# Kernel tuning notes

Hardware: AMD Instinct MI355X
Metric: run time of the kernel (lower is better)

The kernel has to match this reference:

```python
import jax, jax.numpy as jnp
import numpy as np

N_NODES = 50000
N_EDGES = 800000
F_IN = 128      # n_alleles
HID = 64        # ge_hidden_dim
HEADS = 2       # gat_heads
LAT = 128       # latent_dim
N_PHEN = 50


def setup_inputs() -> dict:
    key = jax.random.key(0)
    ks = jax.random.split(key, 16)
    s = 0.05
    return {
        'x': jax.random.normal(ks[0], (N_NODES, F_IN), jnp.float32),
        'edge_index': jax.random.randint(ks[1], (2, N_EDGES), 0, N_NODES, jnp.int64),
        'pheno_idx': jnp.arange(N_PHEN, dtype=jnp.int64),
        'pheno_embedding': jax.random.normal(ks[2], (N_PHEN, F_IN), jnp.float32) * 0.1,
        'Wl1': jax.random.normal(ks[3], (F_IN, HEADS * HID), jnp.float32) * s,
        'Wr1': jax.random.normal(ks[4], (F_IN, HEADS * HID), jnp.float32) * s,
        'att1': jax.random.normal(ks[5], (HEADS, HID), jnp.float32) * s,
        'b1': jax.random.normal(ks[6], (HEADS * HID,), jnp.float32) * s,
        'Wl2': jax.random.normal(ks[7], (HEADS * HID, LAT), jnp.float32) * s,
        'Wr2': jax.random.normal(ks[8], (HEADS * HID, LAT), jnp.float32) * s,
        'att2': jax.random.normal(ks[9], (1, LAT), jnp.float32) * s,
        'b2': jax.random.normal(ks[10], (LAT,), jnp.float32) * s,
        'Wp': jax.random.normal(ks[11], (LAT, LAT), jnp.float32) * s,
        'bp': jax.random.normal(ks[12], (LAT,), jnp.float32) * s,
    }


def gatv2_conv(x, src, dst, Wl, Wr, att, bias, concat):
    # PyG GATv2Conv: e = att . leaky_relu(Wl x_src + Wr x_dst, 0.2), softmax over dst
    N = x.shape[0]
    H, C = att.shape
    xl = (x @ Wl).reshape(N, H, C)
    xr = (x @ Wr).reshape(N, H, C)
    feat = jax.nn.leaky_relu(xl[src] + xr[dst], 0.2)         # [E,H,C]
    logits = jnp.einsum('ehc,hc->eh', feat, att)             # [E,H]
    m = jax.ops.segment_max(logits, dst, num_segments=N)     # [N,H]
    ex = jnp.exp(logits - m[dst])
    denom = jax.ops.segment_sum(ex, dst, num_segments=N)
    alpha = ex / denom[dst]                                  # [E,H]
    out = jax.ops.segment_sum(alpha[:, :, None] * xl[src], dst, num_segments=N)
    out = out.reshape(N, H * C) if concat else out.mean(axis=1)
    return out + bias


def reference(x, edge_index, pheno_idx, pheno_embedding,
              Wl1, Wr1, att1, b1, Wl2, Wr2, att2, b2, Wp, bp):
    N = x.shape[0]
    # learnable phenotype node embeddings replace their input features
    x = x.at[pheno_idx].set(pheno_embedding)
    # PyG default: add self loops
    loops = jnp.arange(N, dtype=edge_index.dtype)
    src = jnp.concatenate([edge_index[0], loops])
    dst = jnp.concatenate([edge_index[1], loops])
    h = jax.nn.leaky_relu(gatv2_conv(x, src, dst, Wl1, Wr1, att1, b1, True), 0.01)
    h = gatv2_conv(h, src, dst, Wl2, Wr2, att2, b2, False)
    graph_embedding = h[pheno_idx].mean(axis=0, keepdims=True)  # [1, LAT]
    return graph_embedding @ Wp + bp
```

## Files before the change

kernel.cpp:

```cpp
#include <hip/hip_runtime.h>
#include <hip/hip_fp16.h>
#include <cstdint>

#define F_DIM 128

__device__ __forceinline__ float lrelu(float x, float s) { return x > 0.f ? x : s * x; }

template<int W>
__device__ __forceinline__ float redg(float p) {
  #pragma unroll
  for (int d = 1; d < W; d <<= 1) p += __shfl_xor(p, d);
  return p;
}

__device__ __forceinline__ int cidx(const int* __restrict__ csr, int k, int last) {
  return csr[k <= last ? k : last];
}

__device__ __forceinline__ __half2 shfl_xor_h2(__half2 v, int m) {
  union { __half2 h; int i; } u; u.h = v;
  u.i = __shfl_xor(u.i, m);
  return u.h;
}

typedef _Float16 h2v __attribute__((ext_vector_type(2)));
__device__ __forceinline__ __half2 h2max(__half2 a, __half2 b) {
  union { __half2 h; h2v v; } ua, ub, ur;
  ua.h = a; ub.h = b;
  ur.v = __builtin_elementwise_max(ua.v, ub.v);
  return ur.h;
}

union H2U { __half2 h[2]; uint2 u; };

__global__ void k_init(int* __restrict__ deg, int* __restrict__ rowmap, int N) {
  int i = blockIdx.x * blockDim.x + threadIdx.x;
  if (i < N) { deg[i] = 0; rowmap[i] = -1; }
}

__global__ void k_hist_rowmap(const int* __restrict__ dst, int* __restrict__ deg,
                              const int* __restrict__ pidx, int* __restrict__ rowmap,
                              int E, int P) {
  int e = blockIdx.x * blockDim.x + threadIdx.x;
  if (e < E) atomicAdd(&deg[dst[e]], 1);
  if (e < P) rowmap[pidx[e]] = e;
}

__global__ void k_scan_reduce(const int* __restrict__ deg, int* __restrict__ bsum, int N) {
  __shared__ int ts[256];
  int tid = threadIdx.x;
  int base = blockIdx.x * 1024 + tid * 4;
  int s = 0;
  #pragma unroll
  for (int j = 0; j < 4; ++j) { int idx = base + j; if (idx < N) s += deg[idx]; }
  ts[tid] = s; __syncthreads();
  for (int d = 128; d > 0; d >>= 1) { if (tid < d) ts[tid] += ts[tid + d]; __syncthreads(); }
  if (tid == 0) bsum[blockIdx.x] = ts[0];
}

__global__ void k_scan_single(int* __restrict__ bsum, int nb) {
  int l = threadIdx.x;
  int v = (l < nb) ? bsum[l] : 0;
  int orig = v;
  #pragma unroll
  for (int d = 1; d < 64; d <<= 1) { int t = __shfl_up(v, d); if (l >= d) v += t; }
  if (l < nb) bsum[l] = v - orig;
}

__global__ void k_scan_final(const int* __restrict__ deg, const int* __restrict__ bsum,
                             int* __restrict__ rowStart, int* __restrict__ cursor,
                             int N, int E) {
  __shared__ int ts[256];
  int tid = threadIdx.x;
  int base = blockIdx.x * 1024 + tid * 4;
  int v[4]; int s = 0;
  #pragma unroll
  for (int j = 0; j < 4; ++j) { int idx = base + j; v[j] = (idx < N) ? deg[idx] : 0; s += v[j]; }
  ts[tid] = s; __syncthreads();
  for (int d = 1; d < 256; d <<= 1) {
    int t = (tid >= d) ? ts[tid - d] : 0;
    __syncthreads();
    ts[tid] += t;
    __syncthreads();
  }
  int off = bsum[blockIdx.x] + ts[tid] - s;
  #pragma unroll
  for (int j = 0; j < 4; ++j) {
    int idx = base + j;
    if (idx < N) { rowStart[idx] = off; cursor[idx] = off; }
    off += v[j];
  }
  if (blockIdx.x == 0 && tid == 0) rowStart[N] = E;
}

__global__ void k_scatter_edges(const int* __restrict__ src, const int* __restrict__ dst,
                                int* __restrict__ cur, int* __restrict__ csr, int E) {
  int e = blockIdx.x * blockDim.x + threadIdx.x;
  if (e >= E) return;
  int d = dst[e];
  int p = atomicAdd(&cur[d], 1);
  csr[p] = src[e];
}

template<bool REMAP>
__global__ __launch_bounds__(256) void k_gemm_dual(
    const float* __restrict__ A, const float* __restrict__ pe, const int* __restrict__ rowmap,
    const float* __restrict__ Wl, const float* __restrict__ Wr,
    __half* __restrict__ outL, __half* __restrict__ outR, int M)
{
  __shared__ float xs[32][68];
  __shared__ float bs[32][256];
  const int tid = threadIdx.x;
  const int m0 = blockIdx.x * 64;
  const int r0 = (tid >> 5) * 8;
  const int cL = (tid & 31) * 4;
  float accL[8][4] = {};
  float accR[8][4] = {};
  for (int k0 = 0; k0 < 128; k0 += 32) {
    #pragma unroll
    for (int i = 0; i < 2; ++i) {
      int q = tid + i * 256;
      int row = q >> 3, qk = q & 7;
      int gr = m0 + row; if (gr > M - 1) gr = M - 1;
      const float* rp = &A[(size_t)gr * 128];
      if (REMAP) {
        int rm = rowmap[gr];
        if (rm >= 0) rp = &pe[(size_t)rm * 128];
      }
      float4 v = *reinterpret_cast<const float4*>(&rp[k0 + qk * 4]);
      xs[qk * 4 + 0][row] = v.x;
      xs[qk * 4 + 1][row] = v.y;
      xs[qk * 4 + 2][row] = v.z;
      xs[qk * 4 + 3][row] = v.w;
    }
    #pragma unroll
    for (int i = 0; i < 4; ++i) {
      int q = tid + i * 256;
      int row = q >> 5, qc = q & 31;
      *reinterpret_cast<float4*>(&bs[row][qc * 4]) =
          *reinterpret_cast<const float4*>(&Wl[(k0 + row) * 128 + qc * 4]);
      *reinterpret_cast<float4*>(&bs[row][128 + qc * 4]) =
          *reinterpret_cast<const float4*>(&Wr[(k0 + row) * 128 + qc * 4]);
    }
    __syncthreads();
    #pragma unroll
    for (int k = 0; k < 32; ++k) {
      float a[8], bL[4], bR[4];
      *reinterpret_cast<float4*>(&a[0]) = *reinterpret_cast<const float4*>(&xs[k][r0]);
      *reinterpret_cast<float4*>(&a[4]) = *reinterpret_cast<const float4*>(&xs[k][r0 + 4]);
      *reinterpret_cast<float4*>(&bL[0]) = *reinterpret_cast<const float4*>(&bs[k][cL]);
      *reinterpret_cast<float4*>(&bR[0]) = *reinterpret_cast<const float4*>(&bs[k][128 + cL]);
      #pragma unroll
      for (int r = 0; r < 8; ++r) {
        #pragma unroll
        for (int c = 0; c < 4; ++c) {
          accL[r][c] = fmaf(a[r], bL[c], accL[r][c]);
          accR[r][c] = fmaf(a[r], bR[c], accR[r][c]);
        }
      }
    }
    __syncthreads();
  }
  #pragma unroll
  for (int r = 0; r < 8; ++r) {
    int gr = m0 + r0 + r;
    if (gr < M) {
      H2U cl, cr;
      cl.h[0] = __float22half2_rn(make_float2(accL[r][0], accL[r][1]));
      cl.h[1] = __float22half2_rn(make_float2(accL[r][2], accL[r][3]));
      cr.h[0] = __float22half2_rn(make_float2(accR[r][0], accR[r][1]));
      cr.h[1] = __float22half2_rn(make_float2(accR[r][2], accR[r][3]));
      *reinterpret_cast<uint2*>(&outL[(size_t)gr * 128 + cL]) = cl.u;
      *reinterpret_cast<uint2*>(&outR[(size_t)gr * 128 + cL]) = cr.u;
    }
  }
}

template<int RW, bool OUTER_LRELU>
__global__ __launch_bounds__(64) void k_agg(
    const __half* __restrict__ xl, const __half* __restrict__ xr,
    const float* __restrict__ att, const float* __restrict__ bias,
    const int* __restrict__ rowStart, const int* __restrict__ csr,
    float* __restrict__ out, int N)
{
  int n = blockIdx.x;
  int l = threadIdx.x;
  int slot = l >> 4;
  int q = l & 15;
  int ch = q * 8;
  size_t nb = (size_t)n * F_DIM + ch;

  float4 rawr = *reinterpret_cast<const float4*>(&xr[nb]);
  float4 rawl = *reinterpret_cast<const float4*>(&xl[nb]);
  const __half2* xrn = reinterpret_cast<const __half2*>(&rawr);
  const __half2* xln = reinterpret_cast<const __half2*>(&rawl);
  __half2 av[4];
  #pragma unroll
  for (int i = 0; i < 4; ++i)
    av[i] = __float22half2_rn(*reinterpret_cast<const float2*>(&att[ch + 2 * i]));
  const __half2 slope = __float2half2_rn(0.2f);

  float denom;
  __half2 acc[4];
  {
    __half2 pr = __float2half2_rn(0.f);
    #pragma unroll
    for (int i = 0; i < 4; ++i) {
      __half2 t = __hadd2(xln[i], xrn[i]);
      __half2 lr = h2max(t, __hmul2(t, slope));
      pr = __hfma2(lr, av[i], pr);
    }
    float2 pf = __half22float2(pr);
    float p = redg<RW>(pf.x + pf.y);
    float w = (slot == 0) ? __expf(p) : 0.f;
    denom = w;
    __half2 wh = __float2half2_rn(w);
    #pragma unroll
    for (int i = 0; i < 4; ++i) acc[i] = __hmul2(xln[i], wh);
  }

  int e0 = rowStart[n], e1 = rowStart[n + 1];
  int last = e1 - 1;
  if (e0 < e1) {
    auto ld = [&](int k) {
      int s = cidx(csr, k, last);
      return *reinterpret_cast<const float4*>(&xl[(size_t)s * F_DIM + ch]);
    };
    auto proc = [&](float4 rawv, int ebase) {
      const __half2* xv = reinterpret_cast<const __half2*>(&rawv);
      __half2 pr = __float2half2_rn(0.f);
      #pragma unroll
      for (int i = 0; i < 4; ++i) {
        __half2 t = __hadd2(xv[i], xrn[i]);
        __half2 lr = h2max(t, __hmul2(t, slope));
        pr = __hfma2(lr, av[i], pr);
      }
      float2 pf = __half22float2(pr);
      float p = redg<RW>(pf.x + pf.y);
      float wE = ((ebase + slot) <= last) ? __expf(p) : 0.f;
      denom += wE;
      __half2 wh = __float2half2_rn(wE);
      #pragma unroll
      for (int i = 0; i < 4; ++i) acc[i] = __hfma2(xv[i], wh, acc[i]);
    };
    float4 v0 = ld(e0 + slot);
    float4 v1 = ld(e0 + 4 + slot);
    for (int e = e0; e < e1; e += 4) {
      bool m2 = (e + 8) < e1;
      float4 v2;
      if (m2) v2 = ld(e + 8 + slot);
      proc(v0, e);
      v0 = v1;
      if (m2) v1 = v2;
    }
  }

  denom += __shfl_xor(denom, 16);
  denom += __shfl_xor(denom, 32);
  #pragma unroll
  for (int i = 0; i < 4; ++i) {
    acc[i] = __hadd2(acc[i], shfl_xor_h2(acc[i], 16));
    acc[i] = __hadd2(acc[i], shfl_xor_h2(acc[i], 32));
  }

  if (slot == 0) {
    float inv = 1.0f / denom;
    float o[8];
    #pragma unroll
    for (int i = 0; i < 4; ++i) {
      float2 a2 = __half22float2(acc[i]);
      o[2 * i + 0] = fmaf(a2.x, inv, bias[ch + 2 * i + 0]);
      o[2 * i + 1] = fmaf(a2.y, inv, bias[ch + 2 * i + 1]);
    }
    if (OUTER_LRELU) {
      #pragma unroll
      for (int i = 0; i < 8; ++i) o[i] = lrelu(o[i], 0.01f);
    }
    *reinterpret_cast<float4*>(&out[nb]) = *reinterpret_cast<float4*>(&o[0]);
    *reinterpret_cast<float4*>(&out[nb + 4]) = *reinterpret_cast<float4*>(&o[4]);
  }
}

__global__ void k_final(const float* __restrict__ h2, const int* __restrict__ pidx,
                        const float* __restrict__ Wp, const float* __restrict__ bp,
                        float* __restrict__ out, int P)
{
  __shared__ float ge[F_DIM];
  int t = threadIdx.x;
  float s0 = 0.f, s1 = 0.f;
  for (int i = 0; i + 1 < P; i += 2) {
    s0 += h2[(size_t)pidx[i] * F_DIM + t];
    s1 += h2[(size_t)pidx[i + 1] * F_DIM + t];
  }
  if (P & 1) s0 += h2[(size_t)pidx[P - 1] * F_DIM + t];
  ge[t] = (s0 + s1) / (float)P;
  __syncthreads();
  float a0 = 0.f, a1 = 0.f, a2 = 0.f, a3 = 0.f;
  for (int k = 0; k < F_DIM; k += 4) {
    a0 = fmaf(ge[k + 0], Wp[(k + 0) * F_DIM + t], a0);
    a1 = fmaf(ge[k + 1], Wp[(k + 1) * F_DIM + t], a1);
    a2 = fmaf(ge[k + 2], Wp[(k + 2) * F_DIM + t], a2);
    a3 = fmaf(ge[k + 3], Wp[(k + 3) * F_DIM + t], a3);
  }
  out[t] = bp[t] + ((a0 + a1) + (a2 + a3));
}

extern "C" void kernel_launch(void* const* d_in, const int* in_sizes, int n_in,
                              void* d_out, int out_size, void* d_ws, size_t ws_size,
                              hipStream_t stream)
{
  const float* x    = (const float*)d_in[0];
  const int*   ei   = (const int*)d_in[1];
  const int*   pidx = (const int*)d_in[2];
  const float* pe   = (const float*)d_in[3];
  const float* Wl1  = (const float*)d_in[4];
  const float* Wr1  = (const float*)d_in[5];
  const float* att1 = (const float*)d_in[6];
  const float* b1   = (const float*)d_in[7];
  const float* Wl2  = (const float*)d_in[8];
  const float* Wr2  = (const float*)d_in[9];
  const float* att2 = (const float*)d_in[10];
  const float* b2   = (const float*)d_in[11];
  const float* Wp   = (const float*)d_in[12];
  const float* bp   = (const float*)d_in[13];
  float* outp = (float*)d_out;

  const int N = in_sizes[0] / F_DIM;
  const int E = in_sizes[1] / 2;
  const int P = in_sizes[2];
  const int* esrc = ei;
  const int* edst = ei + E;

  char* w = (char*)d_ws;
  size_t off = 0;
  auto alloc = [&](size_t bytes) -> void* {
    void* p = w + off;
    off += (bytes + 255) & ~(size_t)255;
    return p;
  };
  const size_t NF = (size_t)N * F_DIM * sizeof(float);
  float*  A  = (float*)alloc(NF);
  __half* Bh = (__half*)alloc(NF / 2);
  __half* Ch = (__half*)alloc(NF / 2);
  int* rowStart = (int*)alloc((size_t)(N + 1) * sizeof(int));
  int* cursor   = (int*)alloc((size_t)N * sizeof(int));
  int* deg      = (int*)alloc((size_t)N * sizeof(int));
  int* bsum     = (int*)alloc(64 * sizeof(int));
  int* rowmap   = (int*)alloc((size_t)N * sizeof(int));
  int* csr      = (int*)alloc((size_t)E * sizeof(int));

  const int nb = (N + 1023) / 1024;

  k_init<<<(N + 255) / 256, 256, 0, stream>>>(deg, rowmap, N);
  k_hist_rowmap<<<(E + 255) / 256, 256, 0, stream>>>(edst, deg, pidx, rowmap, E, P);
  k_scan_reduce<<<nb, 256, 0, stream>>>(deg, bsum, N);
  k_scan_single<<<1, 64, 0, stream>>>(bsum, nb);
  k_scan_final<<<nb, 256, 0, stream>>>(deg, bsum, rowStart, cursor, N, E);
  k_scatter_edges<<<(E + 255) / 256, 256, 0, stream>>>(esrc, edst, cursor, csr, E);

  k_gemm_dual<true><<<(N + 63) / 64, 256, 0, stream>>>(x, pe, rowmap, Wl1, Wr1, Bh, Ch, N);
  k_agg<8, true><<<N, 64, 0, stream>>>(Bh, Ch, att1, b1, rowStart, csr, A, N);
  k_gemm_dual<false><<<(N + 63) / 64, 256, 0, stream>>>(A, nullptr, nullptr, Wl2, Wr2, Bh, Ch, N);
  k_agg<16, false><<<N, 64, 0, stream>>>(Bh, Ch, att2, b2, rowStart, csr, A, N);
  k_final<<<1, 128, 0, stream>>>(A, pidx, Wp, bp, outp, P);
}
```

Baseline: 371.4 us.

## Replace FP32 SIMT dual GEMM with FP16 MFMA GEMM and half-precision activations

Swaps the FP32 shared-memory dual GEMM for a matrix-core kernel that uses 16x16x32 f16 MFMA, reading operands straight from global memory with no LDS staging. The input features and weights are first converted to FP16 in separate kernels, with the weights transposed into one combined Wl|Wr layout. Layer-1 aggregation now writes its output in FP16, so the second GEMM reads half the bytes. The aim is to cut GEMM compute time and memory traffic, at the cost of extra conversion passes, scalar 2-byte output stores, and lower precision on the layer-1 activations.

```diff
diff --git a/kernel.cpp b/kernel.cpp
--- a/kernel.cpp
+++ b/kernel.cpp
@@ -3,6 +3,9 @@
 #include <cstdint>
 
 #define F_DIM 128
+
+typedef _Float16 f16x8 __attribute__((ext_vector_type(8)));
+typedef float f32x4 __attribute__((ext_vector_type(4)));
 
 __device__ __forceinline__ float lrelu(float x, float s) { return x > 0.f ? x : s * x; }
 
@@ -30,8 +33,6 @@
   ur.v = __builtin_elementwise_max(ua.v, ub.v);
   return ur.h;
 }
-
-union H2U { __half2 h[2]; uint2 u; };
 
 __global__ void k_init(int* __restrict__ deg, int* __restrict__ rowmap, int N) {
   int i = blockIdx.x * blockDim.x + threadIdx.x;
@@ -102,86 +103,92 @@
   csr[p] = src[e];
 }
 
-template<bool REMAP>
-__global__ __launch_bounds__(256) void k_gemm_dual(
-    const float* __restrict__ A, const float* __restrict__ pe, const int* __restrict__ rowmap,
-    const float* __restrict__ Wl, const float* __restrict__ Wr,
+__global__ void k_cvt_x(const float* __restrict__ x, const float* __restrict__ pe,
+                        const int* __restrict__ rowmap, __half* __restrict__ xh, int N) {
+  int t = blockIdx.x * 256 + threadIdx.x;
+  if (t >= N * 16) return;
+  int row = t >> 4, seg = (t & 15) * 8;
+  const float* src = &x[(size_t)row * 128 + seg];
+  int rm = rowmap[row];
+  if (rm >= 0) src = &pe[(size_t)rm * 128 + seg];
+  float4 v0 = *reinterpret_cast<const float4*>(src);
+  float4 v1 = *reinterpret_cast<const float4*>(src + 4);
+  union { __half h[8]; float4 f; } pk;
+  pk.h[0] = __float2half(v0.x); pk.h[1] = __float2half(v0.y);
+  pk.h[2] = __float2half(v0.z); pk.h[3] = __float2half(v0.w);
+  pk.h[4] = __float2half(v1.x); pk.h[5] = __float2half(v1.y);
+  pk.h[6] = __float2half(v1.z); pk.h[7] = __float2half(v1.w);
+  *reinterpret_cast<float4*>(&xh[(size_t)row * 128 + seg]) = pk.f;
+}
+
+__global__ void k_cvt_w(const float* __restrict__ Wl1, const float* __restrict__ Wr1,
+                        const float* __restrict__ Wl2, const float* __restrict__ Wr2,
+                        __half* __restrict__ Wt1, __half* __restrict__ Wt2) {
+  int t = blockIdx.x * 256 + threadIdx.x;
+  if (t >= 2 * 32768) return;
+  int layer = t >> 15;
+  int i = t & 32767;
+  int c = i >> 7, k = i & 127;
+  const float* Wl = layer ? Wl2 : Wl1;
+  const float* Wr = layer ? Wr2 : Wr1;
+  float v = (c < 128) ? Wl[k * 128 + c] : Wr[k * 128 + (c - 128)];
+  (layer ? Wt2 : Wt1)[i] = __float2half(v);
+}
+
+__global__ __launch_bounds__(256) void k_gemm_mfma(
+    const __half* __restrict__ Ah, const __half* __restrict__ Wt,
     __half* __restrict__ outL, __half* __restrict__ outR, int M)
 {
-  __shared__ float xs[32][68];
-  __shared__ float bs[32][256];
-  const int tid = threadIdx.x;
-  const int m0 = blockIdx.x * 64;
-  const int r0 = (tid >> 5) * 8;
-  const int cL = (tid & 31) * 4;
-  float accL[8][4] = {};
-  float accR[8][4] = {};
-  for (int k0 = 0; k0 < 128; k0 += 32) {
-    #pragma unroll
-    for (int i = 0; i < 2; ++i) {
-      int q = tid + i * 256;
-      int row = q >> 3, qk = q & 7;
-      int gr = m0 + row; if (gr > M - 1) gr = M - 1;
-      const float* rp = &A[(size_t)gr * 128];
-      if (REMAP) {
-        int rm = rowmap[gr];
-        if (rm >= 0) rp = &pe[(size_t)rm * 128];
-      }
-      float4 v = *reinterpret_cast<const float4*>(&rp[k0 + qk * 4]);
-      xs[qk * 4 + 0][row] = v.x;
-      xs[qk * 4 + 1][row] = v.y;
-      xs[qk * 4 + 2][row] = v.z;
-      xs[qk * 4 + 3][row] = v.w;
-    }
-    #pragma unroll
-    for (int i = 0; i < 4; ++i) {
-      int q = tid + i * 256;
-      int row = q >> 5, qc = q & 31;
-      *reinterpret_cast<float4*>(&bs[row][qc * 4]) =
-          *reinterpret_cast<const float4*>(&Wl[(k0 + row) * 128 + qc * 4]);
-      *reinterpret_cast<float4*>(&bs[row][128 + qc * 4]) =
-          *reinterpret_cast<const float4*>(&Wr[(k0 + row) * 128 + qc * 4]);
-    }
-    __syncthreads();
-    #pragma unroll
-    for (int k = 0; k < 32; ++k) {
-      float a[8], bL[4], bR[4];
-      *reinterpret_cast<float4*>(&a[0]) = *reinterpret_cast<const float4*>(&xs[k][r0]);
-      *reinterpret_cast<float4*>(&a[4]) = *reinterpret_cast<const float4*>(&xs[k][r0 + 4]);
-      *reinterpret_cast<float4*>(&bL[0]) = *reinterpret_cast<const float4*>(&bs[k][cL]);
-      *reinterpret_cast<float4*>(&bR[0]) = *reinterpret_cast<const float4*>(&bs[k][128 + cL]);
-      #pragma unroll
-      for (int r = 0; r < 8; ++r) {
+  int cg = blockIdx.x & 3;
+  int rg = blockIdx.x >> 2;
+  int wv = threadIdx.x >> 6;
+  int l  = threadIdx.x & 63;
+  int rowb = rg * 128 + wv * 32;
+  int colb = cg * 64;
+  int lr = l & 15;
+  int lq = l >> 4;
+  f32x4 acc[2][4] = {};
+  #pragma unroll
+  for (int ks = 0; ks < 4; ++ks) {
+    int k0 = ks * 32 + lq * 8;
+    int r0 = rowb + lr;      if (r0 > M - 1) r0 = M - 1;
+    int r1 = rowb + 16 + lr; if (r1 > M - 1) r1 = M - 1;
+    f16x8 a0 = *reinterpret_cast<const f16x8*>(&Ah[(size_t)r0 * 128 + k0]);
+    f16x8 a1 = *reinterpret_cast<const f16x8*>(&Ah[(size_t)r1 * 128 + k0]);
+    f16x8 b[4];
+    #pragma unroll
+    for (int c = 0; c < 4; ++c)
+      b[c] = *reinterpret_cast<const f16x8*>(&Wt[(size_t)(colb + c * 16 + lr) * 128 + k0]);
+    #pragma unroll
+    for (int c = 0; c < 4; ++c) {
+      acc[0][c] = __builtin_amdgcn_mfma_f32_16x16x32_f16(a0, b[c], acc[0][c], 0, 0, 0);
+      acc[1][c] = __builtin_amdgcn_mfma_f32_16x16x32_f16(a1, b[c], acc[1][c], 0, 0, 0);
+    }
+  }
+  #pragma unroll
+  for (int r = 0; r < 2; ++r) {
+    #pragma unroll
+    for (int j = 0; j < 4; ++j) {
+      int grow = rowb + r * 16 + lq * 4 + j;
+      if (grow < M) {
         #pragma unroll
         for (int c = 0; c < 4; ++c) {
-          accL[r][c] = fmaf(a[r], bL[c], accL[r][c]);
-          accR[r][c] = fmaf(a[r], bR[c], accR[r][c]);
+          int gcol = colb + c * 16 + lr;
+          __half v = __float2half(acc[r][c][j]);
+          if (gcol < 128) outL[(size_t)grow * 128 + gcol] = v;
+          else            outR[(size_t)grow * 128 + (gcol - 128)] = v;
         }
       }
     }
-    __syncthreads();
-  }
-  #pragma unroll
-  for (int r = 0; r < 8; ++r) {
-    int gr = m0 + r0 + r;
-    if (gr < M) {
-      H2U cl, cr;
-      cl.h[0] = __float22half2_rn(make_float2(accL[r][0], accL[r][1]));
-      cl.h[1] = __float22half2_rn(make_float2(accL[r][2], accL[r][3]));
-      cr.h[0] = __float22half2_rn(make_float2(accR[r][0], accR[r][1]));
-      cr.h[1] = __float22half2_rn(make_float2(accR[r][2], accR[r][3]));
-      *reinterpret_cast<uint2*>(&outL[(size_t)gr * 128 + cL]) = cl.u;
-      *reinterpret_cast<uint2*>(&outR[(size_t)gr * 128 + cL]) = cr.u;
-    }
-  }
-}
-
-template<int RW, bool OUTER_LRELU>
+  }
+}
+
+template<int RW, bool OUTER_LRELU, bool HOUT>
 __global__ __launch_bounds__(64) void k_agg(
     const __half* __restrict__ xl, const __half* __restrict__ xr,
     const float* __restrict__ att, const float* __restrict__ bias,
     const int* __restrict__ rowStart, const int* __restrict__ csr,
-    float* __restrict__ out, int N)
+    float* __restrict__ outf, __half* __restrict__ outh, int N)
 {
   int n = blockIdx.x;
   int l = threadIdx.x;
@@ -276,8 +283,15 @@
       #pragma unroll
       for (int i = 0; i < 8; ++i) o[i] = lrelu(o[i], 0.01f);
     }
-    *reinterpret_cast<float4*>(&out[nb]) = *reinterpret_cast<float4*>(&o[0]);
-    *reinterpret_cast<float4*>(&out[nb + 4]) = *reinterpret_cast<float4*>(&o[4]);
+    if (HOUT) {
+      union { __half h[8]; float4 f; } pk;
+      #pragma unroll
+      for (int i = 0; i < 8; ++i) pk.h[i] = __float2half(o[i]);
+      *reinterpret_cast<float4*>(&outh[nb]) = pk.f;
+    } else {
+      *reinterpret_cast<float4*>(&outf[nb]) = *reinterpret_cast<float4*>(&o[0]);
+      *reinterpret_cast<float4*>(&outf[nb + 4]) = *reinterpret_cast<float4*>(&o[4]);
+    }
   }
 }
 
@@ -339,9 +353,13 @@
     return p;
   };
   const size_t NF = (size_t)N * F_DIM * sizeof(float);
-  float*  A  = (float*)alloc(NF);
-  __half* Bh = (__half*)alloc(NF / 2);
-  __half* Ch = (__half*)alloc(NF / 2);
+  float*  A   = (float*)alloc(NF);
+  __half* Bh  = (__half*)alloc(NF / 2);
+  __half* Ch  = (__half*)alloc(NF / 2);
+  __half* Xh  = (__half*)alloc(NF / 2);
+  __half* H1h = (__half*)alloc(NF / 2);
+  __half* Wt1 = (__half*)alloc(2 * 32768 * sizeof(__half));
+  __half* Wt2 = Wt1 + 32768;
   int* rowStart = (int*)alloc((size_t)(N + 1) * sizeof(int));
   int* cursor   = (int*)alloc((size_t)N * sizeof(int));
   int* deg      = (int*)alloc((size_t)N * sizeof(int));
@@ -350,6 +368,7 @@
   int* csr      = (int*)alloc((size_t)E * sizeof(int));
 
   const int nb = (N + 1023) / 1024;
+  const int RG = (N + 127) / 128;
 
   k_init<<<(N + 255) / 256, 256, 0, stream>>>(deg, rowmap, N);
   k_hist_rowmap<<<(E + 255) / 256, 256, 0, stream>>>(edst, deg, pidx, rowmap, E, P);
@@ -358,9 +377,14 @@
   k_scan_final<<<nb, 256, 0, stream>>>(deg, bsum, rowStart, cursor, N, E);
   k_scatter_edges<<<(E + 255) / 256, 256, 0, stream>>>(esrc, edst, cursor, csr, E);
 
-  k_gemm_dual<true><<<(N + 63) / 64, 256, 0, stream>>>(x, pe, rowmap, Wl1, Wr1, Bh, Ch, N);
-  k_agg<8, true><<<N, 64, 0, stream>>>(Bh, Ch, att1, b1, rowStart, csr, A, N);
-  k_gemm_dual<false><<<(N + 63) / 64, 256, 0, stream>>>(A, nullptr, nullptr, Wl2, Wr2, Bh, Ch, N);
-  k_agg<16, false><<<N, 64, 0, stream>>>(Bh, Ch, att2, b2, rowStart, csr, A, N);
+  k_cvt_x<<<(N * 16 + 255) / 256, 256, 0, stream>>>(x, pe, rowmap, Xh, N);
+  k_cvt_w<<<256, 256, 0, stream>>>(Wl1, Wr1, Wl2, Wr2, Wt1, Wt2);
+
+  k_gemm_mfma<<<RG * 4, 256, 0, stream>>>(Xh, Wt1, Bh, Ch, N);
+  k_agg<8, true, true><<<N, 64, 0, stream>>>(Bh, Ch, att1, b1, rowStart, csr,
+                                             nullptr, H1h, N);
+  k_gemm_mfma<<<RG * 4, 256, 0, stream>>>(H1h, Wt2, Bh, Ch, N);
+  k_agg<16, false, false><<<N, 64, 0, stream>>>(Bh, Ch, att2, b2, rowStart, csr,
+                                                A, nullptr, N);
   k_final<<<1, 128, 0, stream>>>(A, pidx, Wp, bp, outp, P);
 }
```

Result: faster. 327.0 us (-11.9%).
